# Performance work log

Measured on AMD Instinct MI355X. Metric: run time of the kernel, lower is better.

Reference implementation:

```python
import jax, jax.numpy as jnp
import numpy as np

H = 65  # LSTM units / vocab size
L = 3   # stacked layers (shared weights)

def _lstm_step(x, h, c, W, U, b):
    # Keras LSTMCell gate order: i, f, c(bar), o
    z = x @ W + h @ U + b  # [B, 4H]
    i, f, g, o = jnp.split(z, 4, axis=-1)
    i = jax.nn.sigmoid(i)
    f = jax.nn.sigmoid(f)
    g = jnp.tanh(g)
    o = jax.nn.sigmoid(o)
    c_new = f * c + i * g
    h_new = o * jnp.tanh(c_new)
    return h_new, c_new

def setup_inputs() -> dict:
    key = jax.random.key(0)
    ks = jax.random.split(key, 4)
    B, T = 50, 4096
    x = jax.random.normal(ks[0], (B, T, H), dtype=jnp.float32)
    s = 1.0 / np.sqrt(H)
    W = jax.random.normal(ks[1], (H, 4 * H), dtype=jnp.float32) * s
    U = jax.random.normal(ks[2], (H, 4 * H), dtype=jnp.float32) * s
    b = jnp.zeros((4 * H,), dtype=jnp.float32)
    Wd = jax.random.normal(ks[3], (H, H), dtype=jnp.float32) * s
    bd = jnp.zeros((H,), dtype=jnp.float32)
    return {"x": x, "W": W, "U": U, "b": b, "Wd": Wd, "bd": bd}

def reference(x, W, U, b, Wd, bd):
    B, T, _ = x.shape
    h0 = jnp.zeros((L, B, H), dtype=x.dtype)
    c0 = jnp.zeros((L, B, H), dtype=x.dtype)

    def step(carry, x_t):
        h, c = carry  # each [L, B, H]
        inp = x_t
        hs, cs = [], []
        for l in range(L):  # 3 layers, SAME weights (shared cell object)
            h_l, c_l = _lstm_step(inp, h[l], c[l], W, U, b)
            hs.append(h_l)
            cs.append(c_l)
            inp = h_l
        return (jnp.stack(hs), jnp.stack(cs)), inp  # output = top-layer hidden

    _, ys = jax.lax.scan(step, (h0, c0), jnp.swapaxes(x, 0, 1))  # ys: [T, B, H]
    ys = jnp.swapaxes(ys, 0, 1)  # [B, T, H]
    return ys @ Wd + bd
```

## Files before the change

kernel.cpp:

```cpp
#include <hip/hip_runtime.h>


#define HH    65
#define G4    260
#define TT    4096
#define NB    50
#define BLOCK 512
#define DROWS 64

#define KEEP4(v) asm volatile("" : "+v"(v.x), "+v"(v.y), "+v"(v.z), "+v"(v.w))
#define KEEP(s)  asm volatile("" : "+v"(s))

__device__ __forceinline__ float sigm(float x)  { return 1.0f / (1.0f + __expf(-x)); }
__device__ __forceinline__ float tanha(float x) { float e = __expf(2.0f * x); return 1.0f - 2.0f / (e + 1.0f); }

__device__ __forceinline__ float qsum(float v) {
    int i = __float_as_int(v);
    v += __int_as_float(__builtin_amdgcn_update_dpp(0, i, 0xB1, 0xF, 0xF, true));
    i = __float_as_int(v);
    v += __int_as_float(__builtin_amdgcn_update_dpp(0, i, 0x4E, 0xF, 0xF, true));
    return v;
}

__global__ void __launch_bounds__(BLOCK)
__attribute__((amdgpu_waves_per_eu(2, 2)))
charrnn_rec(const float* __restrict__ x, const float* __restrict__ W,
            const float* __restrict__ U, const float* __restrict__ bv,
            float* __restrict__ out)
{
    __shared__ __align__(16) float s_hin[3][68];
    __shared__ __align__(16) float s_hrec[3][68];
    __shared__ __align__(16) float s_z[3][2][256];
    __shared__ float s_parte[3][2][4];

    const int bat = blockIdx.x;
    const int tid = threadIdx.x;
    const float* xb   = x   + (size_t)bat * TT * HH;
    float*       outb = out + (size_t)bat * TT * HH;

    for (int i = tid; i < 3 * 68; i += BLOCK) { (&s_hin[0][0])[i] = 0.0f; (&s_hrec[0][0])[i] = 0.0f; }

    const int w    = tid & 3;
    const int side = tid >> 8;
    const int qL   = (tid >> 2) & 63;
    const int col0 = qL * 4;
    const float* M = side ? U : W;

    float4 wa0, wa1, wa2, wa3, wb0, wb1, wb2, wb3,
           wc0, wc1, wc2, wc3, wd0, wd1, wd2, wd3;
#define WLD(v, c, q)                                                          \
    do {                                                                      \
        v.x = M[(16 * w + 4 * (q) + 0) * G4 + col0 + (c)];                    \
        v.y = M[(16 * w + 4 * (q) + 1) * G4 + col0 + (c)];                    \
        v.z = M[(16 * w + 4 * (q) + 2) * G4 + col0 + (c)];                    \
        v.w = M[(16 * w + 4 * (q) + 3) * G4 + col0 + (c)];                    \
        KEEP4(v);                                                             \
    } while (0)
    WLD(wa0, 0, 0); WLD(wa1, 0, 1); WLD(wa2, 0, 2); WLD(wa3, 0, 3);
    WLD(wb0, 1, 0); WLD(wb1, 1, 1); WLD(wb2, 1, 2); WLD(wb3, 1, 3);
    WLD(wc0, 2, 0); WLD(wc1, 2, 1); WLD(wc2, 2, 2); WLD(wc3, 2, 3);
    WLD(wd0, 3, 0); WLD(wd1, 3, 1); WLD(wd2, 3, 2); WLD(wd3, 3, 3);
#undef WLD
    float ws0 = (w == 3) ? M[64 * G4 + col0 + 0] : 0.0f; KEEP(ws0);
    float ws1 = (w == 3) ? M[64 * G4 + col0 + 1] : 0.0f; KEEP(ws1);
    float ws2 = (w == 3) ? M[64 * G4 + col0 + 2] : 0.0f; KEEP(ws2);
    float ws3 = (w == 3) ? M[64 * G4 + col0 + 3] : 0.0f; KEEP(ws3);

    const bool isX  = ((tid & 255) < 16);
    const int  colX = 256 + ((tid >> 2) & 3);
    float4 e0, e1, e2, e3;
    float  esc;
#define ELD(v, q)                                                             \
    do {                                                                      \
        v.x = isX ? M[(16 * w + 4 * (q) + 0) * G4 + colX] : 0.0f;             \
        v.y = isX ? M[(16 * w + 4 * (q) + 1) * G4 + colX] : 0.0f;             \
        v.z = isX ? M[(16 * w + 4 * (q) + 2) * G4 + colX] : 0.0f;             \
        v.w = isX ? M[(16 * w + 4 * (q) + 3) * G4 + colX] : 0.0f;             \
        KEEP4(v);                                                             \
    } while (0)
    ELD(e0, 0); ELD(e1, 1); ELD(e2, 2); ELD(e3, 3);
#undef ELD
    esc = (isX && w == 3) ? M[64 * G4 + colX] : 0.0f; KEEP(esc);

    const int  cl = tid / 65, n = tid - (tid / 65) * 65;
    const bool isC = (tid < 195);
    const float bz0 = bv[n], bz1 = bv[65 + n], bz2 = bv[130 + n], bz3 = bv[195 + n];
    float creg = 0.0f;

    const bool isP  = (tid >= 447);
    const int  pidx = tid - 447;
    float cur = 0.0f, nxt = 0.0f;
    if (isP) {
        s_hin[0][pidx] = xb[pidx];
        cur = xb[HH + pidx];
    }
    __syncthreads();

    for (int r = 0; r < TT + 2; ++r) {
        if (isP) {
            const int tn = r + 2;
            nxt = (tn < TT) ? xb[(size_t)tn * HH + pidx] : 0.0f;
        }
#pragma unroll
        for (int l = 0; l < 3; ++l) {
            if ((unsigned)(r - l) < TT) {
                const float* hb = side ? &s_hrec[l][0] : &s_hin[l][0];
                const float4* h4 = (const float4*)(hb + 16 * w);
                const float4 H0 = h4[0], H1 = h4[1], H2 = h4[2], H3 = h4[3];
                const float  h64 = hb[64];
                float a0, a1, a2, a3;
#define COLDOT(acc, p0, p1, p2, p3, ps)                                       \
    {   float u0, u1;                                                         \
        u0 = H0.x * p0.x;           u1 = H0.y * p0.y;                         \
        u0 = fmaf(H0.z, p0.z, u0);  u1 = fmaf(H0.w, p0.w, u1);                \
        u0 = fmaf(H1.x, p1.x, u0);  u1 = fmaf(H1.y, p1.y, u1);                \
        u0 = fmaf(H1.z, p1.z, u0);  u1 = fmaf(H1.w, p1.w, u1);                \
        u0 = fmaf(H2.x, p2.x, u0);  u1 = fmaf(H2.y, p2.y, u1);                \
        u0 = fmaf(H2.z, p2.z, u0);  u1 = fmaf(H2.w, p2.w, u1);                \
        u0 = fmaf(H3.x, p3.x, u0);  u1 = fmaf(H3.y, p3.y, u1);                \
        u0 = fmaf(H3.z, p3.z, u0);  u1 = fmaf(H3.w, p3.w, u1);                \
        u0 = fmaf(h64, ps, u0);                                               \
        acc = u0 + u1; }
                COLDOT(a0, wa0, wa1, wa2, wa3, ws0)
                COLDOT(a1, wb0, wb1, wb2, wb3, ws1)
                COLDOT(a2, wc0, wc1, wc2, wc3, ws2)
                COLDOT(a3, wd0, wd1, wd2, wd3, ws3)
                a0 = qsum(a0); a1 = qsum(a1); a2 = qsum(a2); a3 = qsum(a3);
                if (w == 0)
                    *(float4*)&s_z[l][side][col0] = make_float4(a0, a1, a2, a3);
                if (isX) {
                    float ea;
                    COLDOT(ea, e0, e1, e2, e3, esc)
                    ea = qsum(ea);
                    if (w == 0) s_parte[l][side][(tid >> 2) & 3] = ea;
                }
#undef COLDOT
            }
        }
        __syncthreads();

        if (isC) {
            if ((unsigned)(r - cl) < TT) {
                const float zi = bz0 + s_z[cl][0][n]       + s_z[cl][1][n];
                const float zf = bz1 + s_z[cl][0][65 + n]  + s_z[cl][1][65 + n];
                const float zg = bz2 + s_z[cl][0][130 + n] + s_z[cl][1][130 + n];
                float zo;
                if (n < 61) zo = bz3 + s_z[cl][0][195 + n]   + s_z[cl][1][195 + n];
                else        zo = bz3 + s_parte[cl][0][n - 61] + s_parte[cl][1][n - 61];
                const float ig = sigm(zi), fg = sigm(zf), gg = tanha(zg), og = sigm(zo);
                creg = fmaf(fg, creg, ig * gg);
                const float h = og * tanha(creg);
                s_hrec[cl][n] = h;
                if (cl < 2) s_hin[cl + 1][n] = h;
                else        outb[(size_t)(r - cl) * HH + n] = h;
            }
        }
        if (isP) {
            if (r + 1 < TT) s_hin[0][pidx] = cur;
            cur = nxt;
        }
        __syncthreads();
    }
}

__global__ void __launch_bounds__(256, 1)
dense_head(float* __restrict__ io, const float* __restrict__ Wd, const float* __restrict__ bd)
{
    __shared__ __align__(16) float s_h[DROWS][68];
    __shared__ float s_wd[HH][HH];
    __shared__ float s_bd[HH];

    const int tid = threadIdx.x;
    float* base = io + (size_t)blockIdx.x * DROWS * HH;

    for (int i = tid; i < DROWS * HH; i += 256) {
        const int row = i / HH, k = i - row * HH;
        s_h[row][k] = base[i];
    }
    for (int i = tid; i < HH * HH; i += 256) (&s_wd[0][0])[i] = Wd[i];
    if (tid < HH) s_bd[tid] = bd[tid];
    __syncthreads();

    for (int u = tid; u < DROWS * HH; u += 256) {
        const int row = u / HH, c = u - row * HH;
        const float4* hp = (const float4*)&s_h[row][0];
        float acc = s_bd[c];
#pragma unroll
        for (int k4 = 0; k4 < 16; ++k4) {
            const float4 hv = hp[k4];
            acc = fmaf(hv.x, s_wd[4 * k4 + 0][c], acc);
            acc = fmaf(hv.y, s_wd[4 * k4 + 1][c], acc);
            acc = fmaf(hv.z, s_wd[4 * k4 + 2][c], acc);
            acc = fmaf(hv.w, s_wd[4 * k4 + 3][c], acc);
        }
        acc = fmaf(s_h[row][64], s_wd[64][c], acc);
        base[u] = acc;
    }
}

extern "C" void kernel_launch(void* const* d_in, const int* in_sizes, int n_in,
                              void* d_out, int out_size, void* d_ws, size_t ws_size,
                              hipStream_t stream)
{
    const float* x  = (const float*)d_in[0];
    const float* W  = (const float*)d_in[1];
    const float* U  = (const float*)d_in[2];
    const float* bv = (const float*)d_in[3];
    const float* Wd = (const float*)d_in[4];
    const float* bd = (const float*)d_in[5];
    float* out = (float*)d_out;

    hipLaunchKernelGGL(charrnn_rec, dim3(NB), dim3(BLOCK), 0, stream, x, W, U, bv, out);
    hipLaunchKernelGGL(dense_head, dim3(NB * TT / DROWS), dim3(256), 0, stream, out, Wd, bd);
}
```

Measured before the change: 6.013 ms.

## Split recurrent dot products across 8 lanes with packed FMA in 1024-thread blocks

Doubles the block to 1024 threads so each gate-column dot product is split over 8 lanes instead of 4, each holding 8 weight rows in registers. The partial sums are computed with packed two-wide FMAs and reduced with a three-step DPP butterfly. The goal is a shorter per-timestep serial dot-product chain on the recurrent critical path. In exchange there are more waves to synchronise at each barrier and an extra reduction step.

```diff
diff --git a/kernel.cpp b/kernel.cpp
--- a/kernel.cpp
+++ b/kernel.cpp
@@ -5,25 +5,28 @@
 #define G4    260
 #define TT    4096
 #define NB    50
-#define BLOCK 512
+#define BLOCK 1024
 #define DROWS 64
 
-#define KEEP4(v) asm volatile("" : "+v"(v.x), "+v"(v.y), "+v"(v.z), "+v"(v.w))
-#define KEEP(s)  asm volatile("" : "+v"(s))
+using v2f = __attribute__((ext_vector_type(2))) float;
+#define PKFMA(a, b, c) __builtin_elementwise_fma((a), (b), (c))
+#define KEEP(s) asm volatile("" : "+v"(s))
 
 __device__ __forceinline__ float sigm(float x)  { return 1.0f / (1.0f + __expf(-x)); }
 __device__ __forceinline__ float tanha(float x) { float e = __expf(2.0f * x); return 1.0f - 2.0f / (e + 1.0f); }
 
-__device__ __forceinline__ float qsum(float v) {
+__device__ __forceinline__ float qsum8(float v) {
     int i = __float_as_int(v);
-    v += __int_as_float(__builtin_amdgcn_update_dpp(0, i, 0xB1, 0xF, 0xF, true));
+    v += __int_as_float(__builtin_amdgcn_update_dpp(0, i, 0xB1,  0xF, 0xF, true));
     i = __float_as_int(v);
-    v += __int_as_float(__builtin_amdgcn_update_dpp(0, i, 0x4E, 0xF, 0xF, true));
+    v += __int_as_float(__builtin_amdgcn_update_dpp(0, i, 0x4E,  0xF, 0xF, true));
+    i = __float_as_int(v);
+    v += __int_as_float(__builtin_amdgcn_update_dpp(0, i, 0x141, 0xF, 0xF, true));
     return v;
 }
 
 __global__ void __launch_bounds__(BLOCK)
-__attribute__((amdgpu_waves_per_eu(2, 2)))
+__attribute__((amdgpu_waves_per_eu(4, 4)))
 charrnn_rec(const float* __restrict__ x, const float* __restrict__ W,
             const float* __restrict__ U, const float* __restrict__ bv,
             float* __restrict__ out)
@@ -33,62 +36,61 @@
     __shared__ __align__(16) float s_z[3][2][256];
     __shared__ float s_parte[3][2][4];
 
-    const int bat = blockIdx.x;
-    const int tid = threadIdx.x;
+    const int bat  = blockIdx.x;
+    const int tid  = threadIdx.x;
+    const int lane = tid & 63;
+    const int wv   = tid >> 6;
     const float* xb   = x   + (size_t)bat * TT * HH;
     float*       outb = out + (size_t)bat * TT * HH;
 
     for (int i = tid; i < 3 * 68; i += BLOCK) { (&s_hin[0][0])[i] = 0.0f; (&s_hrec[0][0])[i] = 0.0f; }
 
-    const int w    = tid & 3;
-    const int side = tid >> 8;
-    const int qL   = (tid >> 2) & 63;
-    const int col0 = qL * 4;
+    const int w    = tid & 7;
+    const int qC   = (tid >> 3) & 63;
+    const int col0 = qC * 4;
+    const int side = tid >> 9;
     const float* M = side ? U : W;
 
-    float4 wa0, wa1, wa2, wa3, wb0, wb1, wb2, wb3,
-           wc0, wc1, wc2, wc3, wd0, wd1, wd2, wd3;
+    v2f wa0, wa1, wa2, wa3, wb0, wb1, wb2, wb3,
+        wc0, wc1, wc2, wc3, wd0, wd1, wd2, wd3;
 #define WLD(v, c, q)                                                          \
     do {                                                                      \
-        v.x = M[(16 * w + 4 * (q) + 0) * G4 + col0 + (c)];                    \
-        v.y = M[(16 * w + 4 * (q) + 1) * G4 + col0 + (c)];                    \
-        v.z = M[(16 * w + 4 * (q) + 2) * G4 + col0 + (c)];                    \
-        v.w = M[(16 * w + 4 * (q) + 3) * G4 + col0 + (c)];                    \
-        KEEP4(v);                                                             \
+        float t0 = M[(8 * w + 2 * (q) + 0) * G4 + col0 + (c)];                \
+        float t1 = M[(8 * w + 2 * (q) + 1) * G4 + col0 + (c)];                \
+        KEEP(t0); KEEP(t1);                                                   \
+        v = (v2f){t0, t1};                                                    \
     } while (0)
     WLD(wa0, 0, 0); WLD(wa1, 0, 1); WLD(wa2, 0, 2); WLD(wa3, 0, 3);
     WLD(wb0, 1, 0); WLD(wb1, 1, 1); WLD(wb2, 1, 2); WLD(wb3, 1, 3);
     WLD(wc0, 2, 0); WLD(wc1, 2, 1); WLD(wc2, 2, 2); WLD(wc3, 2, 3);
     WLD(wd0, 3, 0); WLD(wd1, 3, 1); WLD(wd2, 3, 2); WLD(wd3, 3, 3);
 #undef WLD
-    float ws0 = (w == 3) ? M[64 * G4 + col0 + 0] : 0.0f; KEEP(ws0);
-    float ws1 = (w == 3) ? M[64 * G4 + col0 + 1] : 0.0f; KEEP(ws1);
-    float ws2 = (w == 3) ? M[64 * G4 + col0 + 2] : 0.0f; KEEP(ws2);
-    float ws3 = (w == 3) ? M[64 * G4 + col0 + 3] : 0.0f; KEEP(ws3);
-
-    const bool isX  = ((tid & 255) < 16);
-    const int  colX = 256 + ((tid >> 2) & 3);
-    float4 e0, e1, e2, e3;
-    float  esc;
+    float ws0 = (w == 7) ? M[64 * G4 + col0 + 0] : 0.0f; KEEP(ws0);
+    float ws1 = (w == 7) ? M[64 * G4 + col0 + 1] : 0.0f; KEEP(ws1);
+    float ws2 = (w == 7) ? M[64 * G4 + col0 + 2] : 0.0f; KEEP(ws2);
+    float ws3 = (w == 7) ? M[64 * G4 + col0 + 3] : 0.0f; KEEP(ws3);
+
+    const bool isX  = ((wv == 0) || (wv == 9)) && (lane < 32);
+    const int  colX = 256 + ((lane >> 3) & 3);
+    v2f e0, e1, e2, e3;
 #define ELD(v, q)                                                             \
     do {                                                                      \
-        v.x = isX ? M[(16 * w + 4 * (q) + 0) * G4 + colX] : 0.0f;             \
-        v.y = isX ? M[(16 * w + 4 * (q) + 1) * G4 + colX] : 0.0f;             \
-        v.z = isX ? M[(16 * w + 4 * (q) + 2) * G4 + colX] : 0.0f;             \
-        v.w = isX ? M[(16 * w + 4 * (q) + 3) * G4 + colX] : 0.0f;             \
-        KEEP4(v);                                                             \
+        float t0 = isX ? M[(8 * w + 2 * (q) + 0) * G4 + colX] : 0.0f;         \
+        float t1 = isX ? M[(8 * w + 2 * (q) + 1) * G4 + colX] : 0.0f;         \
+        KEEP(t0); KEEP(t1);                                                   \
+        v = (v2f){t0, t1};                                                    \
     } while (0)
     ELD(e0, 0); ELD(e1, 1); ELD(e2, 2); ELD(e3, 3);
 #undef ELD
-    esc = (isX && w == 3) ? M[64 * G4 + colX] : 0.0f; KEEP(esc);
+    float esc = (isX && w == 7) ? M[64 * G4 + colX] : 0.0f; KEEP(esc);
 
     const int  cl = tid / 65, n = tid - (tid / 65) * 65;
     const bool isC = (tid < 195);
     const float bz0 = bv[n], bz1 = bv[65 + n], bz2 = bv[130 + n], bz3 = bv[195 + n];
     float creg = 0.0f;
 
-    const bool isP  = (tid >= 447);
-    const int  pidx = tid - 447;
+    const bool isP  = (tid >= 959);
+    const int  pidx = tid - 959;
     float cur = 0.0f, nxt = 0.0f;
     if (isP) {
         s_hin[0][pidx] = xb[pidx];
@@ -105,36 +107,32 @@
         for (int l = 0; l < 3; ++l) {
             if ((unsigned)(r - l) < TT) {
                 const float* hb = side ? &s_hrec[l][0] : &s_hin[l][0];
-                const float4* h4 = (const float4*)(hb + 16 * w);
-                const float4 H0 = h4[0], H1 = h4[1], H2 = h4[2], H3 = h4[3];
+                const float4* h4 = (const float4*)(hb + 8 * w);
+                const float4 H0 = h4[0], H1 = h4[1];
                 const float  h64 = hb[64];
+                const v2f hA = (v2f){H0.x, H0.y}, hB = (v2f){H0.z, H0.w};
+                const v2f hC = (v2f){H1.x, H1.y}, hD = (v2f){H1.z, H1.w};
                 float a0, a1, a2, a3;
-#define COLDOT(acc, p0, p1, p2, p3, ps)                                       \
-    {   float u0, u1;                                                         \
-        u0 = H0.x * p0.x;           u1 = H0.y * p0.y;                         \
-        u0 = fmaf(H0.z, p0.z, u0);  u1 = fmaf(H0.w, p0.w, u1);                \
-        u0 = fmaf(H1.x, p1.x, u0);  u1 = fmaf(H1.y, p1.y, u1);                \
-        u0 = fmaf(H1.z, p1.z, u0);  u1 = fmaf(H1.w, p1.w, u1);                \
-        u0 = fmaf(H2.x, p2.x, u0);  u1 = fmaf(H2.y, p2.y, u1);                \
-        u0 = fmaf(H2.z, p2.z, u0);  u1 = fmaf(H2.w, p2.w, u1);                \
-        u0 = fmaf(H3.x, p3.x, u0);  u1 = fmaf(H3.y, p3.y, u1);                \
-        u0 = fmaf(H3.z, p3.z, u0);  u1 = fmaf(H3.w, p3.w, u1);                \
-        u0 = fmaf(h64, ps, u0);                                               \
-        acc = u0 + u1; }
-                COLDOT(a0, wa0, wa1, wa2, wa3, ws0)
-                COLDOT(a1, wb0, wb1, wb2, wb3, ws1)
-                COLDOT(a2, wc0, wc1, wc2, wc3, ws2)
-                COLDOT(a3, wd0, wd1, wd2, wd3, ws3)
-                a0 = qsum(a0); a1 = qsum(a1); a2 = qsum(a2); a3 = qsum(a3);
-                if (w == 0)
+#define CD(res, p0, p1, p2, p3, ps)                                           \
+    {   v2f ac = hA * p0;                                                     \
+        ac = PKFMA(hB, p1, ac);                                               \
+        ac = PKFMA(hC, p2, ac);                                               \
+        ac = PKFMA(hD, p3, ac);                                               \
+        res = fmaf(h64, ps, ac.x + ac.y); }
+                CD(a0, wa0, wa1, wa2, wa3, ws0)
+                CD(a1, wb0, wb1, wb2, wb3, ws1)
+                CD(a2, wc0, wc1, wc2, wc3, ws2)
+                CD(a3, wd0, wd1, wd2, wd3, ws3)
+                a0 = qsum8(a0); a1 = qsum8(a1); a2 = qsum8(a2); a3 = qsum8(a3);
+                if ((lane & 7) == 0)
                     *(float4*)&s_z[l][side][col0] = make_float4(a0, a1, a2, a3);
                 if (isX) {
                     float ea;
-                    COLDOT(ea, e0, e1, e2, e3, esc)
-                    ea = qsum(ea);
-                    if (w == 0) s_parte[l][side][(tid >> 2) & 3] = ea;
+                    CD(ea, e0, e1, e2, e3, esc)
+                    ea = qsum8(ea);
+                    if ((lane & 7) == 0) s_parte[l][side][(lane >> 3) & 3] = ea;
                 }
-#undef COLDOT
+#undef CD
             }
         }
         __syncthreads();
@@ -145,7 +143,7 @@
                 const float zf = bz1 + s_z[cl][0][65 + n]  + s_z[cl][1][65 + n];
                 const float zg = bz2 + s_z[cl][0][130 + n] + s_z[cl][1][130 + n];
                 float zo;
-                if (n < 61) zo = bz3 + s_z[cl][0][195 + n]   + s_z[cl][1][195 + n];
+                if (n < 61) zo = bz3 + s_z[cl][0][195 + n]    + s_z[cl][1][195 + n];
                 else        zo = bz3 + s_parte[cl][0][n - 61] + s_parte[cl][1][n - 61];
                 const float ig = sigm(zi), fg = sigm(zf), gg = tanha(zg), og = sigm(zo);
                 creg = fmaf(fg, creg, ig * gg);
```

Measured after the change: 6.721 ms. 1.12x slower.

## Process two batch sequences per block in recurrent LSTM kernel

Applied to the files above, without the earlier changes.

Each block of the recurrent kernel now handles two batch sequences instead of one, so 25 blocks are launched rather than 50. Both sequences reuse the same register-resident weights and share one pair of barriers per step, so barrier cost is spread over twice the work. In exchange, each step's serial critical path roughly doubles in dot products and cell updates, and fewer CUs are in use, so the serial latency per step grows.

```diff
diff --git a/kernel.cpp b/kernel.cpp
--- a/kernel.cpp
+++ b/kernel.cpp
@@ -4,7 +4,7 @@
 #define HH    65
 #define G4    260
 #define TT    4096
-#define NB    50
+#define NBLK  25
 #define BLOCK 512
 #define DROWS 64
 
@@ -28,17 +28,18 @@
             const float* __restrict__ U, const float* __restrict__ bv,
             float* __restrict__ out)
 {
-    __shared__ __align__(16) float s_hin[3][68];
-    __shared__ __align__(16) float s_hrec[3][68];
-    __shared__ __align__(16) float s_z[3][2][256];
-    __shared__ float s_parte[3][2][4];
-
-    const int bat = blockIdx.x;
+    __shared__ __align__(16) float s_hin[2][3][68];
+    __shared__ __align__(16) float s_hrec[2][3][68];
+    __shared__ __align__(16) float s_z[2][3][2][256];
+    __shared__ float s_parte[2][3][2][4];
+
     const int tid = threadIdx.x;
-    const float* xb   = x   + (size_t)bat * TT * HH;
-    float*       outb = out + (size_t)bat * TT * HH;
-
-    for (int i = tid; i < 3 * 68; i += BLOCK) { (&s_hin[0][0])[i] = 0.0f; (&s_hrec[0][0])[i] = 0.0f; }
+    const float* xb0 = x + (size_t)(2 * blockIdx.x)     * TT * HH;
+    const float* xb1 = x + (size_t)(2 * blockIdx.x + 1) * TT * HH;
+    float* outb0 = out + (size_t)(2 * blockIdx.x)     * TT * HH;
+    float* outb1 = out + (size_t)(2 * blockIdx.x + 1) * TT * HH;
+
+    for (int i = tid; i < 2 * 3 * 68; i += BLOCK) { (&s_hin[0][0][0])[i] = 0.0f; (&s_hrec[0][0][0])[i] = 0.0f; }
 
     const int w    = tid & 3;
     const int side = tid >> 8;
@@ -69,7 +70,6 @@
     const bool isX  = ((tid & 255) < 16);
     const int  colX = 256 + ((tid >> 2) & 3);
     float4 e0, e1, e2, e3;
-    float  esc;
 #define ELD(v, q)                                                             \
     do {                                                                      \
         v.x = isX ? M[(16 * w + 4 * (q) + 0) * G4 + colX] : 0.0f;             \
@@ -80,35 +80,29 @@
     } while (0)
     ELD(e0, 0); ELD(e1, 1); ELD(e2, 2); ELD(e3, 3);
 #undef ELD
-    esc = (isX && w == 3) ? M[64 * G4 + colX] : 0.0f; KEEP(esc);
+    float esc = (isX && w == 3) ? M[64 * G4 + colX] : 0.0f; KEEP(esc);
 
     const int  cl = tid / 65, n = tid - (tid / 65) * 65;
     const bool isC = (tid < 195);
     const float bz0 = bv[n], bz1 = bv[65 + n], bz2 = bv[130 + n], bz3 = bv[195 + n];
-    float creg = 0.0f;
-
-    const bool isP  = (tid >= 447);
-    const int  pidx = tid - 447;
+    float cregA = 0.0f, cregB = 0.0f;
+
+    const bool isP  = (tid >= 382);
+    const int  pseq = (tid >= 447) ? 1 : 0;
+    const int  pidx = tid - 382 - 65 * pseq;
+    const float* xbp = pseq ? xb1 : xb0;
     float cur = 0.0f, nxt = 0.0f;
     if (isP) {
-        s_hin[0][pidx] = xb[pidx];
-        cur = xb[HH + pidx];
+        s_hin[pseq][0][pidx] = xbp[pidx];
+        cur = xbp[HH + pidx];
     }
     __syncthreads();
 
     for (int r = 0; r < TT + 2; ++r) {
         if (isP) {
             const int tn = r + 2;
-            nxt = (tn < TT) ? xb[(size_t)tn * HH + pidx] : 0.0f;
-        }
-#pragma unroll
-        for (int l = 0; l < 3; ++l) {
-            if ((unsigned)(r - l) < TT) {
-                const float* hb = side ? &s_hrec[l][0] : &s_hin[l][0];
-                const float4* h4 = (const float4*)(hb + 16 * w);
-                const float4 H0 = h4[0], H1 = h4[1], H2 = h4[2], H3 = h4[3];
-                const float  h64 = hb[64];
-                float a0, a1, a2, a3;
+            nxt = (tn < TT) ? xbp[(size_t)tn * HH + pidx] : 0.0f;
+        }
 #define COLDOT(acc, p0, p1, p2, p3, ps)                                       \
     {   float u0, u1;                                                         \
         u0 = H0.x * p0.x;           u1 = H0.y * p0.y;                         \
@@ -121,42 +115,58 @@
         u0 = fmaf(H3.z, p3.z, u0);  u1 = fmaf(H3.w, p3.w, u1);                \
         u0 = fmaf(h64, ps, u0);                                               \
         acc = u0 + u1; }
-                COLDOT(a0, wa0, wa1, wa2, wa3, ws0)
-                COLDOT(a1, wb0, wb1, wb2, wb3, ws1)
-                COLDOT(a2, wc0, wc1, wc2, wc3, ws2)
-                COLDOT(a3, wd0, wd1, wd2, wd3, ws3)
-                a0 = qsum(a0); a1 = qsum(a1); a2 = qsum(a2); a3 = qsum(a3);
-                if (w == 0)
-                    *(float4*)&s_z[l][side][col0] = make_float4(a0, a1, a2, a3);
-                if (isX) {
-                    float ea;
-                    COLDOT(ea, e0, e1, e2, e3, esc)
-                    ea = qsum(ea);
-                    if (w == 0) s_parte[l][side][(tid >> 2) & 3] = ea;
-                }
+#define SEQA(ss)                                                              \
+    {   const float* hb = side ? &s_hrec[ss][l][0] : &s_hin[ss][l][0];        \
+        const float4* h4 = (const float4*)(hb + 16 * w);                      \
+        const float4 H0 = h4[0], H1 = h4[1], H2 = h4[2], H3 = h4[3];          \
+        const float  h64 = hb[64];                                            \
+        float a0, a1, a2, a3;                                                 \
+        COLDOT(a0, wa0, wa1, wa2, wa3, ws0)                                   \
+        COLDOT(a1, wb0, wb1, wb2, wb3, ws1)                                   \
+        COLDOT(a2, wc0, wc1, wc2, wc3, ws2)                                   \
+        COLDOT(a3, wd0, wd1, wd2, wd3, ws3)                                   \
+        a0 = qsum(a0); a1 = qsum(a1); a2 = qsum(a2); a3 = qsum(a3);           \
+        if (w == 0)                                                           \
+            *(float4*)&s_z[ss][l][side][col0] = make_float4(a0, a1, a2, a3);  \
+        if (isX) {                                                            \
+            float ea;                                                         \
+            COLDOT(ea, e0, e1, e2, e3, esc)                                   \
+            ea = qsum(ea);                                                    \
+            if (w == 0) s_parte[ss][l][side][(tid >> 2) & 3] = ea;            \
+        } }
+#pragma unroll
+        for (int l = 0; l < 3; ++l) {
+            if ((unsigned)(r - l) < TT) {
+                SEQA(0)
+                SEQA(1)
+            }
+        }
+#undef SEQA
 #undef COLDOT
-            }
-        }
         __syncthreads();
 
         if (isC) {
             if ((unsigned)(r - cl) < TT) {
-                const float zi = bz0 + s_z[cl][0][n]       + s_z[cl][1][n];
-                const float zf = bz1 + s_z[cl][0][65 + n]  + s_z[cl][1][65 + n];
-                const float zg = bz2 + s_z[cl][0][130 + n] + s_z[cl][1][130 + n];
-                float zo;
-                if (n < 61) zo = bz3 + s_z[cl][0][195 + n]   + s_z[cl][1][195 + n];
-                else        zo = bz3 + s_parte[cl][0][n - 61] + s_parte[cl][1][n - 61];
-                const float ig = sigm(zi), fg = sigm(zf), gg = tanha(zg), og = sigm(zo);
-                creg = fmaf(fg, creg, ig * gg);
-                const float h = og * tanha(creg);
-                s_hrec[cl][n] = h;
-                if (cl < 2) s_hin[cl + 1][n] = h;
-                else        outb[(size_t)(r - cl) * HH + n] = h;
+#define CELLB(ss, cregv, outbp)                                               \
+    {   const float zi = bz0 + s_z[ss][cl][0][n]       + s_z[ss][cl][1][n];   \
+        const float zf = bz1 + s_z[ss][cl][0][65 + n]  + s_z[ss][cl][1][65 + n];  \
+        const float zg = bz2 + s_z[ss][cl][0][130 + n] + s_z[ss][cl][1][130 + n]; \
+        float zo;                                                             \
+        if (n < 61) zo = bz3 + s_z[ss][cl][0][195 + n]     + s_z[ss][cl][1][195 + n];  \
+        else        zo = bz3 + s_parte[ss][cl][0][n - 61]  + s_parte[ss][cl][1][n - 61]; \
+        const float ig = sigm(zi), fg = sigm(zf), gg = tanha(zg), og = sigm(zo); \
+        cregv = fmaf(fg, cregv, ig * gg);                                     \
+        const float h = og * tanha(cregv);                                    \
+        s_hrec[ss][cl][n] = h;                                                \
+        if (cl < 2) s_hin[ss][cl + 1][n] = h;                                 \
+        else        outbp[(size_t)(r - cl) * HH + n] = h; }
+                CELLB(0, cregA, outb0)
+                CELLB(1, cregB, outb1)
+#undef CELLB
             }
         }
         if (isP) {
-            if (r + 1 < TT) s_hin[0][pidx] = cur;
+            if (r + 1 < TT) s_hin[pseq][0][pidx] = cur;
             cur = nxt;
         }
         __syncthreads();
@@ -210,6 +220,6 @@
     const float* bd = (const float*)d_in[5];
     float* out = (float*)d_out;
 
-    hipLaunchKernelGGL(charrnn_rec, dim3(NB), dim3(BLOCK), 0, stream, x, W, U, bv, out);
-    hipLaunchKernelGGL(dense_head, dim3(NB * TT / DROWS), dim3(256), 0, stream, out, Wd, bd);
-}
+    hipLaunchKernelGGL(charrnn_rec, dim3(NBLK), dim3(BLOCK), 0, stream, x, W, U, bv, out);
+    hipLaunchKernelGGL(dense_head, dim3(50 * TT / DROWS), dim3(256), 0, stream, out, Wd, bd);
+}
```

New measurement: 11.27 ms. 1.88x slower.

## Pack two batch sequences per 1024-thread block in recurrent LSTM kernel

Applied to the files above, without the earlier changes.

Each workgroup now runs two independent batch sequences, one per half of a 1024-thread block, so 25 blocks are launched instead of 50. Shared buffers get an extra sequence index. The waves-per-EU hint rises from 2 to 4. The extra-column threads for the last output gate are moved onto different waves in each half, which looks aimed at spreading that extra work across SIMDs. The goal is to use fewer CUs and to hide per-step latency and barrier stalls by interleaving two sequences. The risk is that each block-wide barrier now waits for twice as many waves, and register pressure under the higher occupancy hint could cause spills.

```diff
diff --git a/kernel.cpp b/kernel.cpp
--- a/kernel.cpp
+++ b/kernel.cpp
@@ -4,8 +4,8 @@
 #define HH    65
 #define G4    260
 #define TT    4096
-#define NB    50
-#define BLOCK 512
+#define NBLK  25
+#define BLOCK 1024
 #define DROWS 64
 
 #define KEEP4(v) asm volatile("" : "+v"(v.x), "+v"(v.y), "+v"(v.z), "+v"(v.w))
@@ -23,26 +23,31 @@
 }
 
 __global__ void __launch_bounds__(BLOCK)
-__attribute__((amdgpu_waves_per_eu(2, 2)))
+__attribute__((amdgpu_waves_per_eu(4, 4)))
 charrnn_rec(const float* __restrict__ x, const float* __restrict__ W,
             const float* __restrict__ U, const float* __restrict__ bv,
             float* __restrict__ out)
 {
-    __shared__ __align__(16) float s_hin[3][68];
-    __shared__ __align__(16) float s_hrec[3][68];
-    __shared__ __align__(16) float s_z[3][2][256];
-    __shared__ float s_parte[3][2][4];
-
-    const int bat = blockIdx.x;
-    const int tid = threadIdx.x;
+    __shared__ __align__(16) float s_hin[2][3][68];
+    __shared__ __align__(16) float s_hrec[2][3][68];
+    __shared__ __align__(16) float s_z[2][3][2][256];
+    __shared__ float s_parte[2][3][2][4];
+
+    const int tid  = threadIdx.x;
+    const int h    = tid >> 9;
+    const int stid = tid & 511;
+    const int lane = tid & 63;
+    const int wvh  = (tid >> 6) & 7;
+
+    const int bat = 2 * blockIdx.x + h;
     const float* xb   = x   + (size_t)bat * TT * HH;
     float*       outb = out + (size_t)bat * TT * HH;
 
-    for (int i = tid; i < 3 * 68; i += BLOCK) { (&s_hin[0][0])[i] = 0.0f; (&s_hrec[0][0])[i] = 0.0f; }
-
-    const int w    = tid & 3;
-    const int side = tid >> 8;
-    const int qL   = (tid >> 2) & 63;
+    for (int i = tid; i < 2 * 3 * 68; i += BLOCK) { (&s_hin[0][0][0])[i] = 0.0f; (&s_hrec[0][0][0])[i] = 0.0f; }
+
+    const int w    = stid & 3;
+    const int side = stid >> 8;
+    const int qL   = (stid >> 2) & 63;
     const int col0 = qL * 4;
     const float* M = side ? U : W;
 
@@ -66,10 +71,10 @@
     float ws2 = (w == 3) ? M[64 * G4 + col0 + 2] : 0.0f; KEEP(ws2);
     float ws3 = (w == 3) ? M[64 * G4 + col0 + 3] : 0.0f; KEEP(ws3);
 
-    const bool isX  = ((tid & 255) < 16);
-    const int  colX = 256 + ((tid >> 2) & 3);
+    const bool isX = (lane < 16) &&
+                     (h == 0 ? (wvh == 1 || wvh == 6) : (wvh == 3 || wvh == 4));
+    const int  colX = 256 + ((lane >> 2) & 3);
     float4 e0, e1, e2, e3;
-    float  esc;
 #define ELD(v, q)                                                             \
     do {                                                                      \
         v.x = isX ? M[(16 * w + 4 * (q) + 0) * G4 + colX] : 0.0f;             \
@@ -80,18 +85,18 @@
     } while (0)
     ELD(e0, 0); ELD(e1, 1); ELD(e2, 2); ELD(e3, 3);
 #undef ELD
-    esc = (isX && w == 3) ? M[64 * G4 + colX] : 0.0f; KEEP(esc);
-
-    const int  cl = tid / 65, n = tid - (tid / 65) * 65;
-    const bool isC = (tid < 195);
+    float esc = (isX && w == 3) ? M[64 * G4 + colX] : 0.0f; KEEP(esc);
+
+    const int  cl = stid / 65, n = stid - (stid / 65) * 65;
+    const bool isC = (stid < 195);
     const float bz0 = bv[n], bz1 = bv[65 + n], bz2 = bv[130 + n], bz3 = bv[195 + n];
     float creg = 0.0f;
 
-    const bool isP  = (tid >= 447);
-    const int  pidx = tid - 447;
+    const bool isP  = (stid >= 447);
+    const int  pidx = stid - 447;
     float cur = 0.0f, nxt = 0.0f;
     if (isP) {
-        s_hin[0][pidx] = xb[pidx];
+        s_hin[h][0][pidx] = xb[pidx];
         cur = xb[HH + pidx];
     }
     __syncthreads();
@@ -104,7 +109,7 @@
 #pragma unroll
         for (int l = 0; l < 3; ++l) {
             if ((unsigned)(r - l) < TT) {
-                const float* hb = side ? &s_hrec[l][0] : &s_hin[l][0];
+                const float* hb = side ? &s_hrec[h][l][0] : &s_hin[h][l][0];
                 const float4* h4 = (const float4*)(hb + 16 * w);
                 const float4 H0 = h4[0], H1 = h4[1], H2 = h4[2], H3 = h4[3];
                 const float  h64 = hb[64];
@@ -127,12 +132,12 @@
                 COLDOT(a3, wd0, wd1, wd2, wd3, ws3)
                 a0 = qsum(a0); a1 = qsum(a1); a2 = qsum(a2); a3 = qsum(a3);
                 if (w == 0)
-                    *(float4*)&s_z[l][side][col0] = make_float4(a0, a1, a2, a3);
+                    *(float4*)&s_z[h][l][side][col0] = make_float4(a0, a1, a2, a3);
                 if (isX) {
                     float ea;
                     COLDOT(ea, e0, e1, e2, e3, esc)
                     ea = qsum(ea);
-                    if (w == 0) s_parte[l][side][(tid >> 2) & 3] = ea;
+                    if ((lane & 3) == 0) s_parte[h][l][side][(lane >> 2) & 3] = ea;
                 }
 #undef COLDOT
             }
@@ -141,22 +146,22 @@
 
         if (isC) {
             if ((unsigned)(r - cl) < TT) {
-                const float zi = bz0 + s_z[cl][0][n]       + s_z[cl][1][n];
-                const float zf = bz1 + s_z[cl][0][65 + n]  + s_z[cl][1][65 + n];
-                const float zg = bz2 + s_z[cl][0][130 + n] + s_z[cl][1][130 + n];
+                const float zi = bz0 + s_z[h][cl][0][n]       + s_z[h][cl][1][n];
+                const float zf = bz1 + s_z[h][cl][0][65 + n]  + s_z[h][cl][1][65 + n];
+                const float zg = bz2 + s_z[h][cl][0][130 + n] + s_z[h][cl][1][130 + n];
                 float zo;
-                if (n < 61) zo = bz3 + s_z[cl][0][195 + n]   + s_z[cl][1][195 + n];
-                else        zo = bz3 + s_parte[cl][0][n - 61] + s_parte[cl][1][n - 61];
+                if (n < 61) zo = bz3 + s_z[h][cl][0][195 + n]    + s_z[h][cl][1][195 + n];
+                else        zo = bz3 + s_parte[h][cl][0][n - 61] + s_parte[h][cl][1][n - 61];
                 const float ig = sigm(zi), fg = sigm(zf), gg = tanha(zg), og = sigm(zo);
                 creg = fmaf(fg, creg, ig * gg);
-                const float h = og * tanha(creg);
-                s_hrec[cl][n] = h;
-                if (cl < 2) s_hin[cl + 1][n] = h;
-                else        outb[(size_t)(r - cl) * HH + n] = h;
+                const float hv = og * tanha(creg);
+                s_hrec[h][cl][n] = hv;
+                if (cl < 2) s_hin[h][cl + 1][n] = hv;
+                else        outb[(size_t)(r - cl) * HH + n] = hv;
             }
         }
         if (isP) {
-            if (r + 1 < TT) s_hin[0][pidx] = cur;
+            if (r + 1 < TT) s_hin[h][0][pidx] = cur;
             cur = nxt;
         }
         __syncthreads();
@@ -210,6 +215,6 @@
     const float* bd = (const float*)d_in[5];
     float* out = (float*)d_out;
 
-    hipLaunchKernelGGL(charrnn_rec, dim3(NB), dim3(BLOCK), 0, stream, x, W, U, bv, out);
-    hipLaunchKernelGGL(dense_head, dim3(NB * TT / DROWS), dim3(256), 0, stream, out, Wd, bd);
-}
+    hipLaunchKernelGGL(charrnn_rec, dim3(NBLK), dim3(BLOCK), 0, stream, x, W, U, bv, out);
+    hipLaunchKernelGGL(dense_head, dim3(50 * TT / DROWS), dim3(256), 0, stream, out, Wd, bd);
+}
```

Result: slower. 10.21 ms (+69.8%).
